# Optimization experiments

Measured on AMD Instinct MI355X. Metric: run time of the kernel, lower is better.

## Reference

```python
import jax, jax.numpy as jnp
import numpy as np

H = 4  # num_heads
LN_EPS = 1e-5


def setup_inputs() -> dict:
    key = jax.random.key(0)
    ks = jax.random.split(key, 6)
    B, N, IN, OUT = 4, 2048, 256, 256
    return {
        "node_feats": jax.random.normal(ks[0], (B, N, IN), dtype=jnp.float32),
        "adj_matrix": jax.random.uniform(ks[1], (B, N, N), dtype=jnp.float32),
        "W_lin": jax.random.normal(ks[2], (IN, OUT), dtype=jnp.float32) * (IN ** -0.5),
        "b_lin": jnp.zeros((OUT,), dtype=jnp.float32),
        "W_q": jax.random.normal(ks[3], (IN, OUT), dtype=jnp.float32) * (IN ** -0.5),
        "W_k": jax.random.normal(ks[4], (IN, OUT), dtype=jnp.float32) * (IN ** -0.5),
        "ln_g": jnp.ones((OUT,), dtype=jnp.float32),
        "ln_b": jnp.zeros((OUT,), dtype=jnp.float32),
    }


def _heads(x, B, N):
    # [B,N,OUT] -> [B,H,N,hd]
    return x.reshape(B, N, H, -1).transpose(0, 2, 1, 3)


def reference(node_feats, adj_matrix, W_lin, b_lin, W_q, W_k, ln_g, ln_b):
    B, N, _ = node_feats.shape
    out_dim = W_lin.shape[1]
    hd = out_dim // H
    scale = hd ** -0.5
    lrelu = lambda z: jax.nn.leaky_relu(z, 0.01)

    X = _heads(lrelu(node_feats @ W_lin + b_lin), B, N)   # [B,H,N,hd]
    q = _heads(lrelu(node_feats @ W_q), B, N)
    k = _heads(lrelu(node_feats @ W_k), B, N)

    att = jax.nn.sigmoid(jnp.einsum('bhxd,bhyd->bhxy', q, k) * scale)
    adj_h = adj_matrix[:, None] * att                     # [B,H,N,N]

    # symmetric degree normalization: D^-1/2 A D^-1/2 (broadcast form of diag_embed matmuls)
    deg = jnp.sum(adj_h, axis=-1)                         # [B,H,N]
    dis = jnp.where(deg > 0, deg ** -0.5, 0.0)
    A = dis[..., :, None] * adj_h * dis[..., None, :]

    Y = jnp.einsum('bhxy,bhyd->bhxd', A, X)
    Y = Y.transpose(0, 2, 1, 3).reshape(B, N, out_dim)

    mu = jnp.mean(Y, axis=-1, keepdims=True)
    var = jnp.mean((Y - mu) ** 2, axis=-1, keepdims=True)
    return (Y - mu) * jax.lax.rsqrt(var + LN_EPS) * ln_g + ln_b
```

## Files before the change

kernel.cpp:

```cpp
#include <hip/hip_runtime.h>
#include <hip/hip_bf16.h>

#define B_   4
#define N_   2048
#define IN_  256
#define OUT_ 256
#define H_   4
#define HD_  64
#define LN_EPS 1e-5f
#define YCD_ 4
#define YCO_ 2

typedef __bf16 bf16x8 __attribute__((ext_vector_type(8)));
typedef float  f32x4  __attribute__((ext_vector_type(4)));
typedef unsigned short u16x8 __attribute__((ext_vector_type(8)));
typedef unsigned int   u32x4 __attribute__((ext_vector_type(4)));

__device__ __forceinline__ unsigned short f2bf(float x) {
    unsigned int u = __float_as_uint(x);
    return (unsigned short)((u + 0x7FFFu + ((u >> 16) & 1u)) >> 16);
}
__device__ __forceinline__ float bf2f(unsigned short u) {
    return __uint_as_float((unsigned int)u << 16);
}
__device__ __forceinline__ unsigned int cvtpk(float lo, float hi) {
    unsigned int r;
    asm("v_cvt_pk_bf16_f32 %0, %1, %2" : "=v"(r) : "v"(lo), "v"(hi));
    return r;
}

__global__ __launch_bounds__(256) void conv_kernel(
    const float* __restrict__ nf, const float* __restrict__ Wl,
    const float* __restrict__ Wq, const float* __restrict__ Wk,
    unsigned short* __restrict__ nfb, unsigned short* __restrict__ Wt)
{
    const int bid = blockIdx.x, tid = threadIdx.x;
    if (bid < 1024) {
        size_t i = ((size_t)bid * 256 + tid) * 8;
        u16x8 o;
        #pragma unroll
        for (int j = 0; j < 8; j++) o[j] = f2bf(nf[i + j]);
        *(u16x8*)&nfb[i] = o;
    } else {
        int t = (bid - 1024) * 256 + tid;
        int z = t >> 16;
        int l = t & 65535;
        int k = l & 255, n = l >> 8;
        const float* W = (z == 0) ? Wl : (z == 1 ? Wq : Wk);
        Wt[(size_t)z * 65536 + n * 256 + k] = f2bf(W[k * 256 + n]);
    }
}

__global__ __launch_bounds__(256) void gemm3_kernel(
    const unsigned short* __restrict__ nfb, const unsigned short* __restrict__ Wt3,
    const float* __restrict__ bl,
    unsigned short* __restrict__ qb, unsigned short* __restrict__ kb,
    unsigned short* __restrict__ Xt)
{
    const int z  = blockIdx.z;
    const int m0 = blockIdx.x * 64, n0 = blockIdx.y * 64;
    const int tid = threadIdx.x, wave = tid >> 6, lane = tid & 63;
    const int lq = lane >> 4, lr = lane & 15;
    const unsigned short* Wt = Wt3 + (size_t)z * 65536;

    f32x4 acc[4] = {};
    #pragma unroll 4
    for (int k0 = 0; k0 < IN_; k0 += 32) {
        bf16x8 af = *(const bf16x8*)&nfb[(size_t)(m0 + wave * 16 + lr) * IN_ + k0 + lq * 8];
        #pragma unroll
        for (int f = 0; f < 4; f++) {
            bf16x8 bfr = *(const bf16x8*)&Wt[(size_t)(n0 + f * 16 + lr) * IN_ + k0 + lq * 8];
            acc[f] = __builtin_amdgcn_mfma_f32_16x16x32_bf16(af, bfr, acc[f], 0, 0, 0);
        }
    }

    #pragma unroll
    for (int f = 0; f < 4; f++) {
        int c = n0 + f * 16 + lr;
        float bias = (z == 0) ? bl[c] : 0.0f;
        #pragma unroll
        for (int r = 0; r < 4; r++) {
            int m = m0 + wave * 16 + lq * 4 + r;
            float v = acc[f][r] + bias;
            v = (v >= 0.f) ? v : 0.01f * v;
            unsigned short bv = f2bf(v);
            if (z == 0) {
                int n = m & (N_ - 1);
                int h = c >> 6, d = c & 63;
                Xt[(((size_t)(m >> 11) * H_ + h) * HD_ + d) * N_ + n] = bv;
            } else {
                unsigned short* dst = (z == 1) ? qb : kb;
                dst[(size_t)m * OUT_ + c] = bv;
            }
        }
    }
}

__global__ __launch_bounds__(256) void deg_kernel(
    const float* __restrict__ adj,
    const unsigned short* __restrict__ qb,
    const unsigned short* __restrict__ kb,
    float* __restrict__ deg)
{
    const int b = blockIdx.y, x0 = blockIdx.x * 16, yc = blockIdx.z;
    const int tid = threadIdx.x, h = tid >> 6, lane = tid & 63;
    const int lq = lane >> 4, lr = lane & 15;
    const float sc = -0.125f * 1.44269504088896f;
    __shared__ __align__(16) float ads[16][68];

    bf16x8 qf[2];
    #pragma unroll
    for (int ks = 0; ks < 2; ks++)
        qf[ks] = *(const bf16x8*)&qb[(size_t)(b * N_ + x0 + lr) * OUT_ + h * HD_ + ks * 32 + lq * 8];

    float degp[4] = {};

    for (int yt = 0; yt < N_ / YCD_ / 64; yt++) {
        const int y0 = yc * (N_ / YCD_) + yt * 64;
        {
            int r = tid >> 4, c = (tid & 15) * 4;
            *(f32x4*)&ads[r][c] = *(const f32x4*)&adj[((size_t)b * N_ + x0 + r) * N_ + y0 + c];
        }
        f32x4 S[4] = {};
        #pragma unroll
        for (int yb = 0; yb < 4; yb++) {
            #pragma unroll
            for (int ks = 0; ks < 2; ks++) {
                bf16x8 kf = *(const bf16x8*)&kb[(size_t)(b * N_ + y0 + yb * 16 + lr) * OUT_ + h * HD_ + ks * 32 + lq * 8];
                S[yb] = __builtin_amdgcn_mfma_f32_16x16x32_bf16(qf[ks], kf, S[yb], 0, 0, 0);
            }
        }
        __syncthreads();
        #pragma unroll
        for (int yb = 0; yb < 4; yb++) {
            #pragma unroll
            for (int r = 0; r < 4; r++) {
                float a = ads[lq * 4 + r][yb * 16 + lr];
                float att = __builtin_amdgcn_rcpf(1.f + exp2f(S[yb][r] * sc));
                degp[r] += a * att;
            }
        }
        __syncthreads();
    }
    #pragma unroll
    for (int r = 0; r < 4; r++) {
        float v = degp[r];
        v += __shfl_xor(v, 1); v += __shfl_xor(v, 2);
        v += __shfl_xor(v, 4); v += __shfl_xor(v, 8);
        degp[r] = v;
    }
    if (lr == 0) {
        #pragma unroll
        for (int r = 0; r < 4; r++)
            atomicAdd(&deg[((size_t)b * H_ + h) * N_ + x0 + lq * 4 + r], degp[r]);
    }
}

__global__ __launch_bounds__(256) void scale_kernel(
    const unsigned short* __restrict__ Xt, const float* __restrict__ deg,
    unsigned short* __restrict__ Xs, float* __restrict__ dis)
{
    const int t = blockIdx.x * 256 + threadIdx.x;
    const size_t idx = (size_t)t * 8;
    const int bh = t >> 14;
    const int y  = (int)(idx & (N_ - 1));
    f32x4 g0 = *(const f32x4*)&deg[bh * N_ + y];
    f32x4 g1 = *(const f32x4*)&deg[bh * N_ + y + 4];
    float dv[8];
    #pragma unroll
    for (int j = 0; j < 4; j++) {
        dv[j]     = (g0[j] > 0.f) ? rsqrtf(g0[j]) : 0.f;
        dv[4 + j] = (g1[j] > 0.f) ? rsqrtf(g1[j]) : 0.f;
    }
    if ((t & 16383) < 256) {
        f32x4 o0 = {dv[0], dv[1], dv[2], dv[3]};
        f32x4 o1 = {dv[4], dv[5], dv[6], dv[7]};
        *(f32x4*)&dis[bh * N_ + y]     = o0;
        *(f32x4*)&dis[bh * N_ + y + 4] = o1;
    }
    u16x8 x = *(const u16x8*)&Xt[idx];
    u32x4 o;
    o[0] = cvtpk(bf2f(x[0]) * dv[0], bf2f(x[1]) * dv[1]);
    o[1] = cvtpk(bf2f(x[2]) * dv[2], bf2f(x[3]) * dv[3]);
    o[2] = cvtpk(bf2f(x[4]) * dv[4], bf2f(x[5]) * dv[5]);
    o[3] = cvtpk(bf2f(x[6]) * dv[6], bf2f(x[7]) * dv[7]);
    *(u32x4*)&Xs[idx] = o;
}

__global__ __launch_bounds__(256) void out1_kernel(
    const float* __restrict__ adj,
    const unsigned short* __restrict__ qb,
    const unsigned short* __restrict__ kb,
    const unsigned short* __restrict__ Xs,
    float* __restrict__ Ypart)
{
    const int b = blockIdx.y, x0 = blockIdx.x * 16, yc = blockIdx.z;
    const int tid = threadIdx.x, h = tid >> 6, lane = tid & 63;
    const int lq = lane >> 4, lr = lane & 15;
    const float sc = -0.125f * 1.44269504088896f;
    __shared__ __align__(16) float ads[16][68];
    __shared__ __align__(16) float wt[4][16][68];

    bf16x8 qf[2];
    #pragma unroll
    for (int ks = 0; ks < 2; ks++)
        qf[ks] = *(const bf16x8*)&qb[(size_t)(b * N_ + x0 + lr) * OUT_ + h * HD_ + ks * 32 + lq * 8];

    f32x4 Y[4] = {};

    for (int yt = 0; yt < N_ / YCO_ / 64; yt++) {
        const int y0 = yc * (N_ / YCO_) + yt * 64;
        {
            int r = tid >> 4, c = (tid & 15) * 4;
            *(f32x4*)&ads[r][c] = *(const f32x4*)&adj[((size_t)b * N_ + x0 + r) * N_ + y0 + c];
        }
        f32x4 S[4] = {};
        #pragma unroll
        for (int yb = 0; yb < 4; yb++) {
            #pragma unroll
            for (int ks = 0; ks < 2; ks++) {
                bf16x8 kf = *(const bf16x8*)&kb[(size_t)(b * N_ + y0 + yb * 16 + lr) * OUT_ + h * HD_ + ks * 32 + lq * 8];
                S[yb] = __builtin_amdgcn_mfma_f32_16x16x32_bf16(qf[ks], kf, S[yb], 0, 0, 0);
            }
        }
        __syncthreads();
        #pragma unroll
        for (int yb = 0; yb < 4; yb++) {
            #pragma unroll
            for (int r = 0; r < 4; r++) {
                float a = ads[lq * 4 + r][yb * 16 + lr];
                float att = __builtin_amdgcn_rcpf(1.f + exp2f(S[yb][r] * sc));
                wt[h][lq * 4 + r][yb * 16 + lr] = a * att;
            }
        }
        #pragma unroll
        for (int ks = 0; ks < 2; ks++) {
            f32x4 w0 = *(const f32x4*)&wt[h][lr][ks * 32 + lq * 8];
            f32x4 w1 = *(const f32x4*)&wt[h][lr][ks * 32 + lq * 8 + 4];
            union { u32x4 u; bf16x8 v; } wu;
            wu.u[0] = cvtpk(w0[0], w0[1]);
            wu.u[1] = cvtpk(w0[2], w0[3]);
            wu.u[2] = cvtpk(w1[0], w1[1]);
            wu.u[3] = cvtpk(w1[2], w1[3]);
            #pragma unroll
            for (int db = 0; db < 4; db++) {
                bf16x8 xf = *(const bf16x8*)&Xs[(((size_t)b * H_ + h) * HD_ + db * 16 + lr) * N_ + y0 + ks * 32 + lq * 8];
                Y[db] = __builtin_amdgcn_mfma_f32_16x16x32_bf16(wu.v, xf, Y[db], 0, 0, 0);
            }
        }
        __syncthreads();
    }

    #pragma unroll
    for (int db = 0; db < 4; db++)
        #pragma unroll
        for (int r = 0; r < 4; r++)
            Ypart[((size_t)(yc * B_ + b) * N_ + x0 + lq * 4 + r) * OUT_ + h * HD_ + db * 16 + lr] = Y[db][r];
}

__global__ __launch_bounds__(256) void out2_kernel(
    const float* __restrict__ Yp, const float* __restrict__ dis,
    const float* __restrict__ lng, const float* __restrict__ lnb,
    float* __restrict__ out)
{
    const int row = blockIdx.x;
    const int c = threadIdx.x;
    const size_t PS = (size_t)B_ * N_ * OUT_;
    const size_t base = (size_t)row * OUT_ + c;
    float v = Yp[base];
    #pragma unroll
    for (int p = 1; p < YCO_; p++) v += Yp[base + (size_t)p * PS];
    const int b = row >> 11, x = row & (N_ - 1);
    v *= dis[((size_t)b * H_ + (c >> 6)) * N_ + x];

    float s1 = v, s2 = v * v;
    #pragma unroll
    for (int d = 1; d < 64; d <<= 1) { s1 += __shfl_xor(s1, d); s2 += __shfl_xor(s2, d); }
    __shared__ float red[2][4];
    if ((c & 63) == 0) { red[0][c >> 6] = s1; red[1][c >> 6] = s2; }
    __syncthreads();
    float t1 = red[0][0] + red[0][1] + red[0][2] + red[0][3];
    float t2 = red[1][0] + red[1][1] + red[1][2] + red[1][3];
    float mu  = t1 * (1.f / 256.f);
    float var = t2 * (1.f / 256.f) - mu * mu;
    float rs  = rsqrtf(var + LN_EPS);
    out[base] = (v - mu) * rs * lng[c] + lnb[c];
}

extern "C" void kernel_launch(void* const* d_in, const int* in_sizes, int n_in,
                              void* d_out, int out_size, void* d_ws, size_t ws_size,
                              hipStream_t stream) {
    const float* nf  = (const float*)d_in[0];
    const float* adj = (const float*)d_in[1];
    const float* Wl  = (const float*)d_in[2];
    const float* bl  = (const float*)d_in[3];
    const float* Wq  = (const float*)d_in[4];
    const float* Wk  = (const float*)d_in[5];
    const float* lng = (const float*)d_in[6];
    const float* lnb = (const float*)d_in[7];
    float* out = (float*)d_out;

    char* w = (char*)d_ws;
    unsigned short* nfb = (unsigned short*)w;  w += (size_t)B_ * N_ * IN_ * 2;
    unsigned short* Wt  = (unsigned short*)w;  w += (size_t)3 * IN_ * OUT_ * 2;
    unsigned short* qb  = (unsigned short*)w;  w += (size_t)B_ * N_ * OUT_ * 2;
    unsigned short* kb  = (unsigned short*)w;  w += (size_t)B_ * N_ * OUT_ * 2;
    unsigned short* Xt  = (unsigned short*)w;  w += (size_t)B_ * N_ * OUT_ * 2;
    unsigned short* Xs  = (unsigned short*)w;  w += (size_t)B_ * N_ * OUT_ * 2;
    float* deg = (float*)w;                    w += (size_t)B_ * H_ * N_ * 4;
    float* dis = (float*)w;                    w += (size_t)B_ * H_ * N_ * 4;
    float* Yp  = (float*)w;                    w += (size_t)YCO_ * B_ * N_ * OUT_ * 4;

    hipMemsetAsync(deg, 0, (size_t)B_ * H_ * N_ * 4, stream);
    conv_kernel <<<1792, 256, 0, stream>>>(nf, Wl, Wq, Wk, nfb, Wt);
    gemm3_kernel<<<dim3(128, 4, 3), 256, 0, stream>>>(nfb, Wt, bl, qb, kb, Xt);
    deg_kernel  <<<dim3(N_ / 16, B_, YCD_), 256, 0, stream>>>(adj, qb, kb, deg);
    scale_kernel<<<1024, 256, 0, stream>>>(Xt, deg, Xs, dis);
    out1_kernel <<<dim3(N_ / 16, B_, YCO_), 256, 0, stream>>>(adj, qb, kb, Xs, Yp);
    out2_kernel <<<B_ * N_, 256, 0, stream>>>(Yp, dis, lng, lnb, out);
}
```

Before: 337.3 us.

## Materialize bf16 attention-weighted adjacency once and reuse it for degree and output GEMM

Replaces the two passes that each recomputed QK^T and the sigmoid and re-read fp32 adj (one for degree, one for output) with a single tiled att_kernel. It writes the weighted adjacency as bf16 to a workspace buffer and emits per-tile degree partials without atomics. A plain bf16 GEMM kernel then consumes this buffer and fuses the D^-1/2 row scaling and LayerNorm, removing the split-K fp32 partial buffer and the separate LN kernel. The cost is a large N*N*16 bf16 intermediate written and read back, plus batching by workspace size, with a fallback to one batch at a time.

```diff
diff --git a/kernel.cpp b/kernel.cpp
--- a/kernel.cpp
+++ b/kernel.cpp
@@ -8,8 +8,6 @@
 #define H_   4
 #define HD_  64
 #define LN_EPS 1e-5f
-#define YCD_ 4
-#define YCO_ 2
 
 typedef __bf16 bf16x8 __attribute__((ext_vector_type(8)));
 typedef float  f32x4  __attribute__((ext_vector_type(4)));
@@ -96,195 +94,181 @@
     }
 }
 
-__global__ __launch_bounds__(256) void deg_kernel(
+__global__ __launch_bounds__(256) void att_kernel(
     const float* __restrict__ adj,
     const unsigned short* __restrict__ qb,
     const unsigned short* __restrict__ kb,
-    float* __restrict__ deg)
-{
-    const int b = blockIdx.y, x0 = blockIdx.x * 16, yc = blockIdx.z;
+    unsigned short* __restrict__ W,
+    float* __restrict__ degp,
+    int b_base, int SH)
+{
+    const int s  = blockIdx.z;
+    const int bg = b_base + (s >> 2);
+    const int hg = s & 3;
+    const int x0 = blockIdx.x * 128, y0 = blockIdx.y * 128;
+    const int tid = threadIdx.x, wave = tid >> 6, lane = tid & 63;
+    const int lq = lane >> 4, lr = lane & 15;
+    const int wq = wave >> 1, wn = wave & 1;
+    const int wx0 = x0 + wq * 64, wy0 = y0 + wn * 64;
+    const float sc = -0.125f * 1.44269504088896f;
+
+    const unsigned short* qrow = qb + (size_t)(bg * N_ + wx0) * OUT_ + hg * HD_;
+    const unsigned short* krow = kb + (size_t)(bg * N_ + wy0) * OUT_ + hg * HD_;
+
+    f32x4 acc[4][4] = {};
+    #pragma unroll
+    for (int ks = 0; ks < 2; ks++) {
+        bf16x8 af[4], bf[4];
+        #pragma unroll
+        for (int mf = 0; mf < 4; mf++)
+            af[mf] = *(const bf16x8*)&qrow[(size_t)(mf * 16 + lr) * OUT_ + ks * 32 + lq * 8];
+        #pragma unroll
+        for (int nf = 0; nf < 4; nf++)
+            bf[nf] = *(const bf16x8*)&krow[(size_t)(nf * 16 + lr) * OUT_ + ks * 32 + lq * 8];
+        #pragma unroll
+        for (int mf = 0; mf < 4; mf++)
+            #pragma unroll
+            for (int nf = 0; nf < 4; nf++)
+                acc[mf][nf] = __builtin_amdgcn_mfma_f32_16x16x32_bf16(af[mf], bf[nf], acc[mf][nf], 0, 0, 0);
+    }
+
+    unsigned short* Wp = W + (size_t)s * N_ * N_;
+    #pragma unroll
+    for (int mf = 0; mf < 4; mf++) {
+        #pragma unroll
+        for (int r = 0; r < 4; r++) {
+            int x = wx0 + mf * 16 + lq * 4 + r;
+            const float* arow = adj + ((size_t)bg * N_ + x) * N_ + wy0;
+            unsigned short* wrow = Wp + (size_t)x * N_ + wy0;
+            float sum = 0.f;
+            #pragma unroll
+            for (int nf = 0; nf < 4; nf++) {
+                float a = arow[nf * 16 + lr];
+                float att = __builtin_amdgcn_rcpf(1.f + exp2f(acc[mf][nf][r] * sc));
+                float wv = a * att;
+                sum += wv;
+                wrow[nf * 16 + lr] = f2bf(wv);
+            }
+            sum += __shfl_xor(sum, 1); sum += __shfl_xor(sum, 2);
+            sum += __shfl_xor(sum, 4); sum += __shfl_xor(sum, 8);
+            if (lr == 0)
+                degp[((size_t)(blockIdx.y * 2 + wn) * SH + s) * N_ + x] = sum;
+        }
+    }
+}
+
+__global__ __launch_bounds__(256) void degsum_kernel(
+    const float* __restrict__ degp, float* __restrict__ dis, int b_base, int SH)
+{
+    int t = blockIdx.x * 256 + threadIdx.x;
+    int s = t >> 11, x = t & (N_ - 1);
+    float sum = 0.f;
+    #pragma unroll
+    for (int j = 0; j < 32; j++) sum += degp[((size_t)j * SH + s) * N_ + x];
+    dis[((size_t)b_base * H_ + s) * N_ + x] = (sum > 0.f) ? rsqrtf(sum) : 0.f;
+}
+
+__global__ __launch_bounds__(256) void scale_kernel(
+    const unsigned short* __restrict__ Xt, const float* __restrict__ dis,
+    unsigned short* __restrict__ Xs)
+{
+    int t = blockIdx.x * 256 + threadIdx.x;
+    size_t idx = (size_t)t * 8;
+    int s = t >> 14;
+    int y = (int)(idx & (N_ - 1));
+    f32x4 d0 = *(const f32x4*)&dis[(size_t)s * N_ + y];
+    f32x4 d1 = *(const f32x4*)&dis[(size_t)s * N_ + y + 4];
+    u16x8 x = *(const u16x8*)&Xt[idx];
+    u32x4 o;
+    o[0] = cvtpk(bf2f(x[0]) * d0[0], bf2f(x[1]) * d0[1]);
+    o[1] = cvtpk(bf2f(x[2]) * d0[2], bf2f(x[3]) * d0[3]);
+    o[2] = cvtpk(bf2f(x[4]) * d1[0], bf2f(x[5]) * d1[1]);
+    o[3] = cvtpk(bf2f(x[6]) * d1[2], bf2f(x[7]) * d1[3]);
+    *(u32x4*)&Xs[idx] = o;
+}
+
+__global__ __launch_bounds__(256) void yout_kernel(
+    const unsigned short* __restrict__ W,
+    const unsigned short* __restrict__ Xs,
+    const float* __restrict__ dis,
+    const float* __restrict__ lng, const float* __restrict__ lnb,
+    float* __restrict__ out, int b_base)
+{
+    const int x0 = blockIdx.x * 16;
+    const int bl = blockIdx.y;
+    const int bg = b_base + bl;
     const int tid = threadIdx.x, h = tid >> 6, lane = tid & 63;
     const int lq = lane >> 4, lr = lane & 15;
-    const float sc = -0.125f * 1.44269504088896f;
-    __shared__ __align__(16) float ads[16][68];
-
-    bf16x8 qf[2];
-    #pragma unroll
-    for (int ks = 0; ks < 2; ks++)
-        qf[ks] = *(const bf16x8*)&qb[(size_t)(b * N_ + x0 + lr) * OUT_ + h * HD_ + ks * 32 + lq * 8];
-
-    float degp[4] = {};
-
-    for (int yt = 0; yt < N_ / YCD_ / 64; yt++) {
-        const int y0 = yc * (N_ / YCD_) + yt * 64;
-        {
-            int r = tid >> 4, c = (tid & 15) * 4;
-            *(f32x4*)&ads[r][c] = *(const f32x4*)&adj[((size_t)b * N_ + x0 + r) * N_ + y0 + c];
-        }
-        f32x4 S[4] = {};
-        #pragma unroll
-        for (int yb = 0; yb < 4; yb++) {
-            #pragma unroll
-            for (int ks = 0; ks < 2; ks++) {
-                bf16x8 kf = *(const bf16x8*)&kb[(size_t)(b * N_ + y0 + yb * 16 + lr) * OUT_ + h * HD_ + ks * 32 + lq * 8];
-                S[yb] = __builtin_amdgcn_mfma_f32_16x16x32_bf16(qf[ks], kf, S[yb], 0, 0, 0);
-            }
-        }
-        __syncthreads();
-        #pragma unroll
-        for (int yb = 0; yb < 4; yb++) {
-            #pragma unroll
-            for (int r = 0; r < 4; r++) {
-                float a = ads[lq * 4 + r][yb * 16 + lr];
-                float att = __builtin_amdgcn_rcpf(1.f + exp2f(S[yb][r] * sc));
-                degp[r] += a * att;
-            }
-        }
-        __syncthreads();
-    }
-    #pragma unroll
-    for (int r = 0; r < 4; r++) {
-        float v = degp[r];
-        v += __shfl_xor(v, 1); v += __shfl_xor(v, 2);
-        v += __shfl_xor(v, 4); v += __shfl_xor(v, 8);
-        degp[r] = v;
-    }
-    if (lr == 0) {
-        #pragma unroll
-        for (int r = 0; r < 4; r++)
-            atomicAdd(&deg[((size_t)b * H_ + h) * N_ + x0 + lq * 4 + r], degp[r]);
-    }
-}
-
-__global__ __launch_bounds__(256) void scale_kernel(
-    const unsigned short* __restrict__ Xt, const float* __restrict__ deg,
-    unsigned short* __restrict__ Xs, float* __restrict__ dis)
-{
-    const int t = blockIdx.x * 256 + threadIdx.x;
-    const size_t idx = (size_t)t * 8;
-    const int bh = t >> 14;
-    const int y  = (int)(idx & (N_ - 1));
-    f32x4 g0 = *(const f32x4*)&deg[bh * N_ + y];
-    f32x4 g1 = *(const f32x4*)&deg[bh * N_ + y + 4];
-    float dv[8];
-    #pragma unroll
-    for (int j = 0; j < 4; j++) {
-        dv[j]     = (g0[j] > 0.f) ? rsqrtf(g0[j]) : 0.f;
-        dv[4 + j] = (g1[j] > 0.f) ? rsqrtf(g1[j]) : 0.f;
-    }
-    if ((t & 16383) < 256) {
-        f32x4 o0 = {dv[0], dv[1], dv[2], dv[3]};
-        f32x4 o1 = {dv[4], dv[5], dv[6], dv[7]};
-        *(f32x4*)&dis[bh * N_ + y]     = o0;
-        *(f32x4*)&dis[bh * N_ + y + 4] = o1;
-    }
-    u16x8 x = *(const u16x8*)&Xt[idx];
-    u32x4 o;
-    o[0] = cvtpk(bf2f(x[0]) * dv[0], bf2f(x[1]) * dv[1]);
-    o[1] = cvtpk(bf2f(x[2]) * dv[2], bf2f(x[3]) * dv[3]);
-    o[2] = cvtpk(bf2f(x[4]) * dv[4], bf2f(x[5]) * dv[5]);
-    o[3] = cvtpk(bf2f(x[6]) * dv[6], bf2f(x[7]) * dv[7]);
-    *(u32x4*)&Xs[idx] = o;
-}
-
-__global__ __launch_bounds__(256) void out1_kernel(
-    const float* __restrict__ adj,
-    const unsigned short* __restrict__ qb,
-    const unsigned short* __restrict__ kb,
-    const unsigned short* __restrict__ Xs,
-    float* __restrict__ Ypart)
-{
-    const int b = blockIdx.y, x0 = blockIdx.x * 16, yc = blockIdx.z;
-    const int tid = threadIdx.x, h = tid >> 6, lane = tid & 63;
-    const int lq = lane >> 4, lr = lane & 15;
-    const float sc = -0.125f * 1.44269504088896f;
-    __shared__ __align__(16) float ads[16][68];
-    __shared__ __align__(16) float wt[4][16][68];
-
-    bf16x8 qf[2];
-    #pragma unroll
-    for (int ks = 0; ks < 2; ks++)
-        qf[ks] = *(const bf16x8*)&qb[(size_t)(b * N_ + x0 + lr) * OUT_ + h * HD_ + ks * 32 + lq * 8];
+    const int s = bl * H_ + h;
+
+    const unsigned short* Wp = W + (size_t)s * N_ * N_ + (size_t)(x0 + lr) * N_;
+    const unsigned short* Xp = Xs + ((size_t)s * HD_ + lr) * N_;
 
     f32x4 Y[4] = {};
-
-    for (int yt = 0; yt < N_ / YCO_ / 64; yt++) {
-        const int y0 = yc * (N_ / YCO_) + yt * 64;
-        {
-            int r = tid >> 4, c = (tid & 15) * 4;
-            *(f32x4*)&ads[r][c] = *(const f32x4*)&adj[((size_t)b * N_ + x0 + r) * N_ + y0 + c];
-        }
-        f32x4 S[4] = {};
-        #pragma unroll
-        for (int yb = 0; yb < 4; yb++) {
-            #pragma unroll
-            for (int ks = 0; ks < 2; ks++) {
-                bf16x8 kf = *(const bf16x8*)&kb[(size_t)(b * N_ + y0 + yb * 16 + lr) * OUT_ + h * HD_ + ks * 32 + lq * 8];
-                S[yb] = __builtin_amdgcn_mfma_f32_16x16x32_bf16(qf[ks], kf, S[yb], 0, 0, 0);
-            }
-        }
-        __syncthreads();
-        #pragma unroll
-        for (int yb = 0; yb < 4; yb++) {
-            #pragma unroll
-            for (int r = 0; r < 4; r++) {
-                float a = ads[lq * 4 + r][yb * 16 + lr];
-                float att = __builtin_amdgcn_rcpf(1.f + exp2f(S[yb][r] * sc));
-                wt[h][lq * 4 + r][yb * 16 + lr] = a * att;
-            }
-        }
+    for (int k0 = 0; k0 < N_; k0 += 64) {
         #pragma unroll
         for (int ks = 0; ks < 2; ks++) {
-            f32x4 w0 = *(const f32x4*)&wt[h][lr][ks * 32 + lq * 8];
-            f32x4 w1 = *(const f32x4*)&wt[h][lr][ks * 32 + lq * 8 + 4];
-            union { u32x4 u; bf16x8 v; } wu;
-            wu.u[0] = cvtpk(w0[0], w0[1]);
-            wu.u[1] = cvtpk(w0[2], w0[3]);
-            wu.u[2] = cvtpk(w1[0], w1[1]);
-            wu.u[3] = cvtpk(w1[2], w1[3]);
+            bf16x8 af = *(const bf16x8*)&Wp[k0 + ks * 32 + lq * 8];
             #pragma unroll
             for (int db = 0; db < 4; db++) {
-                bf16x8 xf = *(const bf16x8*)&Xs[(((size_t)b * H_ + h) * HD_ + db * 16 + lr) * N_ + y0 + ks * 32 + lq * 8];
-                Y[db] = __builtin_amdgcn_mfma_f32_16x16x32_bf16(wu.v, xf, Y[db], 0, 0, 0);
+                bf16x8 xf = *(const bf16x8*)&Xp[(size_t)db * 16 * N_ + k0 + ks * 32 + lq * 8];
+                Y[db] = __builtin_amdgcn_mfma_f32_16x16x32_bf16(af, xf, Y[db], 0, 0, 0);
             }
         }
-        __syncthreads();
-    }
-
-    #pragma unroll
-    for (int db = 0; db < 4; db++)
-        #pragma unroll
-        for (int r = 0; r < 4; r++)
-            Ypart[((size_t)(yc * B_ + b) * N_ + x0 + lq * 4 + r) * OUT_ + h * HD_ + db * 16 + lr] = Y[db][r];
-}
-
-__global__ __launch_bounds__(256) void out2_kernel(
-    const float* __restrict__ Yp, const float* __restrict__ dis,
-    const float* __restrict__ lng, const float* __restrict__ lnb,
-    float* __restrict__ out)
-{
-    const int row = blockIdx.x;
-    const int c = threadIdx.x;
-    const size_t PS = (size_t)B_ * N_ * OUT_;
-    const size_t base = (size_t)row * OUT_ + c;
-    float v = Yp[base];
-    #pragma unroll
-    for (int p = 1; p < YCO_; p++) v += Yp[base + (size_t)p * PS];
-    const int b = row >> 11, x = row & (N_ - 1);
-    v *= dis[((size_t)b * H_ + (c >> 6)) * N_ + x];
-
-    float s1 = v, s2 = v * v;
-    #pragma unroll
-    for (int d = 1; d < 64; d <<= 1) { s1 += __shfl_xor(s1, d); s2 += __shfl_xor(s2, d); }
-    __shared__ float red[2][4];
-    if ((c & 63) == 0) { red[0][c >> 6] = s1; red[1][c >> 6] = s2; }
+    }
+
+    float dx[4];
+    #pragma unroll
+    for (int r = 0; r < 4; r++)
+        dx[r] = dis[((size_t)bg * H_ + h) * N_ + x0 + lq * 4 + r];
+
+    __shared__ float lnred[2][4][16];
+    float s1[4] = {}, s2[4] = {};
+    #pragma unroll
+    for (int r = 0; r < 4; r++) {
+        #pragma unroll
+        for (int db = 0; db < 4; db++) {
+            float v = Y[db][r] * dx[r];
+            s1[r] += v; s2[r] += v * v;
+        }
+    }
+    #pragma unroll
+    for (int r = 0; r < 4; r++) {
+        float a = s1[r], q2 = s2[r];
+        a += __shfl_xor(a, 1); a += __shfl_xor(a, 2); a += __shfl_xor(a, 4); a += __shfl_xor(a, 8);
+        q2 += __shfl_xor(q2, 1); q2 += __shfl_xor(q2, 2); q2 += __shfl_xor(q2, 4); q2 += __shfl_xor(q2, 8);
+        s1[r] = a; s2[r] = q2;
+    }
+    if (lr == 0) {
+        #pragma unroll
+        for (int r = 0; r < 4; r++) {
+            lnred[0][h][lq * 4 + r] = s1[r];
+            lnred[1][h][lq * 4 + r] = s2[r];
+        }
+    }
     __syncthreads();
-    float t1 = red[0][0] + red[0][1] + red[0][2] + red[0][3];
-    float t2 = red[1][0] + red[1][1] + red[1][2] + red[1][3];
-    float mu  = t1 * (1.f / 256.f);
-    float var = t2 * (1.f / 256.f) - mu * mu;
-    float rs  = rsqrtf(var + LN_EPS);
-    out[base] = (v - mu) * rs * lng[c] + lnb[c];
+
+    float gg[4], bb[4];
+    #pragma unroll
+    for (int db = 0; db < 4; db++) {
+        int c = h * HD_ + db * 16 + lr;
+        gg[db] = lng[c]; bb[db] = lnb[c];
+    }
+    #pragma unroll
+    for (int r = 0; r < 4; r++) {
+        int xr = lq * 4 + r;
+        float t1 = lnred[0][0][xr] + lnred[0][1][xr] + lnred[0][2][xr] + lnred[0][3][xr];
+        float t2 = lnred[1][0][xr] + lnred[1][1][xr] + lnred[1][2][xr] + lnred[1][3][xr];
+        float mu  = t1 * (1.f / 256.f);
+        float var = t2 * (1.f / 256.f) - mu * mu;
+        float rs  = rsqrtf(var + LN_EPS);
+        #pragma unroll
+        for (int db = 0; db < 4; db++) {
+            int c = h * HD_ + db * 16 + lr;
+            float v = (Y[db][r] * dx[r] - mu) * rs * gg[db] + bb[db];
+            out[((size_t)(bg * N_ + x0 + xr)) * OUT_ + c] = v;
+        }
+    }
 }
 
 extern "C" void kernel_launch(void* const* d_in, const int* in_sizes, int n_in,
@@ -307,15 +291,23 @@
     unsigned short* kb  = (unsigned short*)w;  w += (size_t)B_ * N_ * OUT_ * 2;
     unsigned short* Xt  = (unsigned short*)w;  w += (size_t)B_ * N_ * OUT_ * 2;
     unsigned short* Xs  = (unsigned short*)w;  w += (size_t)B_ * N_ * OUT_ * 2;
-    float* deg = (float*)w;                    w += (size_t)B_ * H_ * N_ * 4;
     float* dis = (float*)w;                    w += (size_t)B_ * H_ * N_ * 4;
-    float* Yp  = (float*)w;                    w += (size_t)YCO_ * B_ * N_ * OUT_ * 4;
-
-    hipMemsetAsync(deg, 0, (size_t)B_ * H_ * N_ * 4, stream);
+    size_t fixed = (size_t)(w - (char*)d_ws);
+
+    size_t need4 = fixed + (size_t)32 * 16 * N_ * 4 + (size_t)16 * N_ * N_ * 2;
+    int nb = (ws_size >= need4) ? 4 : 1;
+    int SH = nb * H_;
+    float* degp = (float*)w;                   w += (size_t)32 * SH * N_ * 4;
+    unsigned short* Wbuf = (unsigned short*)w;
+
     conv_kernel <<<1792, 256, 0, stream>>>(nf, Wl, Wq, Wk, nfb, Wt);
     gemm3_kernel<<<dim3(128, 4, 3), 256, 0, stream>>>(nfb, Wt, bl, qb, kb, Xt);
-    deg_kernel  <<<dim3(N_ / 16, B_, YCD_), 256, 0, stream>>>(adj, qb, kb, deg);
-    scale_kernel<<<1024, 256, 0, stream>>>(Xt, deg, Xs, dis);
-    out1_kernel <<<dim3(N_ / 16, B_, YCO_), 256, 0, stream>>>(adj, qb, kb, Xs, Yp);
-    out2_kernel <<<B_ * N_, 256, 0, stream>>>(Yp, dis, lng, lnb, out);
-}
+
+    for (int b0 = 0; b0 < B_; b0 += nb) {
+        size_t xoff = (size_t)b0 * H_ * HD_ * N_;
+        att_kernel   <<<dim3(16, 16, SH), 256, 0, stream>>>(adj, qb, kb, Wbuf, degp, b0, SH);
+        degsum_kernel<<<SH * N_ / 256, 256, 0, stream>>>(degp, dis, b0, SH);
+        scale_kernel <<<SH * HD_ * N_ / 8 / 256, 256, 0, stream>>>(Xt + xoff, dis + (size_t)b0 * H_ * N_, Xs + xoff);
+        yout_kernel  <<<dim3(N_ / 16, nb), 256, 0, stream>>>(Wbuf, Xs + xoff, dis, lng, lnb, out, b0);
+    }
+}
```

Result: faster. 315.3 us (-6.5%).
